# Kernel tuning notes

Hardware: AMD Instinct MI355X
Metric: run time of the kernel (lower is better)

The kernel has to match this reference:

```python
import jax, jax.numpy as jnp
import numpy as np


def setup_inputs() -> dict:
    key = jax.random.key(0)
    k1, k2, k3 = jax.random.split(key, 3)
    B, N, L, H, E = 4, 4, 1024, 8, 64
    queries = jax.random.normal(k1, (B, N, L, H, E), dtype=jnp.float32)
    keys = jax.random.normal(k2, (B, N, L, H, E), dtype=jnp.float32)
    values = jax.random.normal(k3, (B, N, L, H, E), dtype=jnp.float32)
    return {"queries": queries, "keys": keys, "values": values}


def reference(queries, keys, values):
    B, N, L, H, E = queries.shape
    S = values.shape[2]
    scale = 1.0 / jnp.sqrt(jnp.asarray(E, queries.dtype))
    # scores: [B, N, H, L, S]
    scores = jnp.einsum('bnlhe,bnshe->bnhls', queries, keys)
    # causal mask: True above the diagonal (future positions), broadcast over b,n,h
    causal = jnp.triu(jnp.ones((L, S), dtype=bool), k=1)
    scores = jnp.where(causal, -jnp.inf, scores)
    A = jax.nn.softmax(scale * scores, axis=-1)  # dropout p=0.0 -> identity
    V = jnp.einsum('bnhls,bnshd->bnlhd', A, values)
    return V
```

## Files before the change

### kernel.cpp

```cpp
#include <hip/hip_runtime.h>
#include <hip/hip_bf16.h>


typedef __bf16 bf16x8 __attribute__((ext_vector_type(8)));
typedef __bf16 bf16x4 __attribute__((ext_vector_type(4)));
typedef float  f32x4  __attribute__((ext_vector_type(4)));

#define SEQ 1024
#define ROWSTRIDE 512
#define LDSPAD 72

__device__ inline bf16x8 pack8(float4 a, float4 b) {
    bf16x8 f;
    f[0]=(__bf16)a.x; f[1]=(__bf16)a.y; f[2]=(__bf16)a.z; f[3]=(__bf16)a.w;
    f[4]=(__bf16)b.x; f[5]=(__bf16)b.y; f[6]=(__bf16)b.z; f[7]=(__bf16)b.w;
    return f;
}

__device__ inline bf16x8 pack8s(float4 a, float4 b, float s) {
    bf16x8 f;
    f[0]=(__bf16)(a.x*s); f[1]=(__bf16)(a.y*s); f[2]=(__bf16)(a.z*s); f[3]=(__bf16)(a.w*s);
    f[4]=(__bf16)(b.x*s); f[5]=(__bf16)(b.y*s); f[6]=(__bf16)(b.z*s); f[7]=(__bf16)(b.w*s);
    return f;
}

__device__ inline void lds_barrier() {
    asm volatile("s_waitcnt lgkmcnt(0)\n\ts_barrier" ::: "memory");
}

__global__ __launch_bounds__(256) void attn_fwd(
    const float* __restrict__ Qg,
    const float* __restrict__ Kg,
    const float* __restrict__ Vg,
    float* __restrict__ Og)
{
    __shared__ __bf16 Kds[64][LDSPAD];
    __shared__ __bf16 Vds[64][LDSPAD];
    __shared__ __bf16 Pds[2][4][16][LDSPAD];

    const int blk  = blockIdx.x;
    const int pr   = blk >> 7;
    const int head = blk & 127;
    const int h    = head & 7;
    const int bn   = head >> 3;
    const int qts[2] = { pr, 15 - pr };

    const int tid  = threadIdx.x;
    const int wave = tid >> 6;
    const int lane = tid & 63;
    const int quad = lane >> 4;
    const int l15  = lane & 15;

    const size_t base = (size_t)bn * SEQ * ROWSTRIDE + (size_t)h * 64;

    const float kscale = 0.125f * 1.44269504088896f;

    bf16x8 qa[2][2];
    int qrow[2];
    #pragma unroll
    for (int st = 0; st < 2; ++st) {
        qrow[st] = qts[st] * 64 + wave * 16;
        const float* qp = Qg + base + (size_t)(qrow[st] + l15) * ROWSTRIDE + quad * 8;
        #pragma unroll
        for (int t = 0; t < 2; ++t)
            qa[st][t] = pack8s(*(const float4*)(qp + t * 32),
                               *(const float4*)(qp + t * 32 + 4), kscale);
    }

    f32x4 o[2][4];
    float lsum[2];
    #pragma unroll
    for (int st = 0; st < 2; ++st) {
        #pragma unroll
        for (int e = 0; e < 4; ++e) o[st][e] = (f32x4){0.f, 0.f, 0.f, 0.f};
        lsum[st] = 0.f;
    }

    const int sr = tid >> 2, sc = (tid & 3) << 4;
    const int ve = tid & 63, vs = (tid >> 6) << 4;

    const int ntiles = qts[1] + 1;

    const float* kbase = Kg + base;
    const float* vbase = Vg + base;

    float4 kpre[4];
    float  vpre[16];
    {
        const float* kp = kbase + (size_t)sr * ROWSTRIDE + sc;
        #pragma unroll
        for (int i = 0; i < 4; ++i) kpre[i] = *(const float4*)(kp + i * 4);
        const float* vp = vbase + (size_t)vs * ROWSTRIDE + ve;
        #pragma unroll
        for (int j = 0; j < 16; ++j) vpre[j] = vp[(size_t)j * ROWSTRIDE];
    }

    for (int tile = 0; tile < ntiles; ++tile) {
        lds_barrier();

        *(bf16x8*)&Kds[sr][sc]     = pack8(kpre[0], kpre[1]);
        *(bf16x8*)&Kds[sr][sc + 8] = pack8(kpre[2], kpre[3]);
        {
            bf16x8 f0, f1;
            #pragma unroll
            for (int jj = 0; jj < 8; ++jj) { f0[jj] = (__bf16)vpre[jj]; f1[jj] = (__bf16)vpre[8 + jj]; }
            *(bf16x8*)&Vds[ve][vs]     = f0;
            *(bf16x8*)&Vds[ve][vs + 8] = f1;
        }

        if (tile + 1 < ntiles) {
            const int s0n = (tile + 1) * 64;
            const float* kp = kbase + (size_t)(s0n + sr) * ROWSTRIDE + sc;
            #pragma unroll
            for (int i = 0; i < 4; ++i) kpre[i] = *(const float4*)(kp + i * 4);
            const float* vp = vbase + (size_t)(s0n + vs) * ROWSTRIDE + ve;
            #pragma unroll
            for (int j = 0; j < 16; ++j) vpre[j] = vp[(size_t)j * ROWSTRIDE];
        }

        lds_barrier();

        #pragma unroll
        for (int st = 0; st < 2; ++st) {
            if (tile > qts[st]) continue;
            f32x4 sacc[4];
            #pragma unroll
            for (int c = 0; c < 4; ++c) {
                sacc[c] = (f32x4){0.f, 0.f, 0.f, 0.f};
                #pragma unroll
                for (int t = 0; t < 2; ++t) {
                    bf16x8 kb = *(const bf16x8*)&Kds[c * 16 + l15][t * 32 + quad * 8];
                    sacc[c] = __builtin_amdgcn_mfma_f32_16x16x32_bf16(kb, qa[st][t], sacc[c], 0, 0, 0);
                }
            }
            const bool diag = (tile == qts[st]);
            const int qin = wave * 16 + l15;
            float ls = 0.f;
            #pragma unroll
            for (int c = 0; c < 4; ++c) {
                bf16x4 pk;
                #pragma unroll
                for (int r = 0; r < 4; ++r) {
                    float p = __builtin_amdgcn_exp2f(sacc[c][r]);
                    if (diag && (c * 16 + quad * 4 + r > qin)) p = 0.f;
                    ls += p;
                    pk[r] = (__bf16)p;
                }
                *(bf16x4*)&Pds[st][wave][l15][c * 16 + quad * 4] = pk;
            }
            lsum[st] += ls;
        }

        asm volatile("s_waitcnt lgkmcnt(0)" ::: "memory");

        const bool both = (tile <= qts[0]);
        #pragma unroll
        for (int e = 0; e < 4; ++e) {
            #pragma unroll
            for (int t = 0; t < 2; ++t) {
                bf16x8 vb = *(const bf16x8*)&Vds[e * 16 + l15][t * 32 + quad * 8];
                if (both) {
                    bf16x8 pb0 = *(const bf16x8*)&Pds[0][wave][l15][t * 32 + quad * 8];
                    o[0][e] = __builtin_amdgcn_mfma_f32_16x16x32_bf16(vb, pb0, o[0][e], 0, 0, 0);
                }
                bf16x8 pb1 = *(const bf16x8*)&Pds[1][wave][l15][t * 32 + quad * 8];
                o[1][e] = __builtin_amdgcn_mfma_f32_16x16x32_bf16(vb, pb1, o[1][e], 0, 0, 0);
            }
        }
    }

    #pragma unroll
    for (int st = 0; st < 2; ++st) {
        float s = lsum[st];
        s += __shfl_xor(s, 16);
        s += __shfl_xor(s, 32);
        const float inv_l = 1.f / s;
        float* op = Og + base + (size_t)(qrow[st] + l15) * ROWSTRIDE + quad * 4;
        #pragma unroll
        for (int e = 0; e < 4; ++e) {
            float4 v;
            v.x = o[st][e][0] * inv_l;
            v.y = o[st][e][1] * inv_l;
            v.z = o[st][e][2] * inv_l;
            v.w = o[st][e][3] * inv_l;
            *(float4*)(op + e * 16) = v;
        }
    }
}

extern "C" void kernel_launch(void* const* d_in, const int* in_sizes, int n_in,
                              void* d_out, int out_size, void* d_ws, size_t ws_size,
                              hipStream_t stream) {
    const float* Qg = (const float*)d_in[0];
    const float* Kg = (const float*)d_in[1];
    const float* Vg = (const float*)d_in[2];
    float* Og = (float*)d_out;
    attn_fwd<<<dim3(1024), dim3(256), 0, stream>>>(Qg, Kg, Vg, Og);
}
```

Measured before the change: 163.5 us.

## Keep P in registers, double-buffer swizzled K/V LDS, use 16x16x16 MFMA for PV

```diff
diff --git a/kernel.cpp b/kernel.cpp
--- a/kernel.cpp
+++ b/kernel.cpp
@@ -5,10 +5,10 @@
 typedef __bf16 bf16x8 __attribute__((ext_vector_type(8)));
 typedef __bf16 bf16x4 __attribute__((ext_vector_type(4)));
 typedef float  f32x4  __attribute__((ext_vector_type(4)));
+typedef short  s16x4  __attribute__((ext_vector_type(4)));
 
 #define SEQ 1024
 #define ROWSTRIDE 512
-#define LDSPAD 72
 
 __device__ inline bf16x8 pack8(float4 a, float4 b) {
     bf16x8 f;
@@ -28,15 +28,14 @@
     asm volatile("s_waitcnt lgkmcnt(0)\n\ts_barrier" ::: "memory");
 }
 
-__global__ __launch_bounds__(256) void attn_fwd(
+__global__ __launch_bounds__(256, 4) void attn_fwd(
     const float* __restrict__ Qg,
     const float* __restrict__ Kg,
     const float* __restrict__ Vg,
     float* __restrict__ Og)
 {
-    __shared__ __bf16 Kds[64][LDSPAD];
-    __shared__ __bf16 Vds[64][LDSPAD];
-    __shared__ __bf16 Pds[2][4][16][LDSPAD];
+    __shared__ __bf16 Kds[2][64][64];
+    __shared__ __bf16 Vds[2][64][64];
 
     const int blk  = blockIdx.x;
     const int pr   = blk >> 7;
@@ -50,6 +49,7 @@
     const int lane = tid & 63;
     const int quad = lane >> 4;
     const int l15  = lane & 15;
+    const int swz  = l15 & 7;
 
     const size_t base = (size_t)bn * SEQ * ROWSTRIDE + (size_t)h * 64;
 
@@ -76,8 +76,8 @@
         lsum[st] = 0.f;
     }
 
-    const int sr = tid >> 2, sc = (tid & 3) << 4;
-    const int ve = tid & 63, vs = (tid >> 6) << 4;
+    const int sr = tid >> 2, cbk = (tid & 3) << 1;
+    const int ve = tid & 63, cbv = (tid >> 6) << 1;
 
     const int ntiles = qts[1] + 1;
 
@@ -87,39 +87,42 @@
     float4 kpre[4];
     float  vpre[16];
     {
-        const float* kp = kbase + (size_t)sr * ROWSTRIDE + sc;
+        const float* kp = kbase + (size_t)sr * ROWSTRIDE + (cbk << 3);
         #pragma unroll
         for (int i = 0; i < 4; ++i) kpre[i] = *(const float4*)(kp + i * 4);
-        const float* vp = vbase + (size_t)vs * ROWSTRIDE + ve;
+        const float* vp = vbase + (size_t)(cbv << 3) * ROWSTRIDE + ve;
         #pragma unroll
         for (int j = 0; j < 16; ++j) vpre[j] = vp[(size_t)j * ROWSTRIDE];
     }
 
     for (int tile = 0; tile < ntiles; ++tile) {
-        lds_barrier();
+        const int bb = tile & 1;
 
-        *(bf16x8*)&Kds[sr][sc]     = pack8(kpre[0], kpre[1]);
-        *(bf16x8*)&Kds[sr][sc + 8] = pack8(kpre[2], kpre[3]);
         {
+            const int rk = sr & 7;
+            *(bf16x8*)&Kds[bb][sr][(cbk ^ rk) << 3]       = pack8(kpre[0], kpre[1]);
+            *(bf16x8*)&Kds[bb][sr][((cbk + 1) ^ rk) << 3] = pack8(kpre[2], kpre[3]);
             bf16x8 f0, f1;
             #pragma unroll
             for (int jj = 0; jj < 8; ++jj) { f0[jj] = (__bf16)vpre[jj]; f1[jj] = (__bf16)vpre[8 + jj]; }
-            *(bf16x8*)&Vds[ve][vs]     = f0;
-            *(bf16x8*)&Vds[ve][vs + 8] = f1;
+            const int rv = ve & 7;
+            *(bf16x8*)&Vds[bb][ve][(cbv ^ rv) << 3]       = f0;
+            *(bf16x8*)&Vds[bb][ve][((cbv + 1) ^ rv) << 3] = f1;
         }
 
         if (tile + 1 < ntiles) {
-            const int s0n = (tile + 1) * 64;
-            const float* kp = kbase + (size_t)(s0n + sr) * ROWSTRIDE + sc;
+            const int s0n = (tile + 1) << 6;
+            const float* kp = kbase + (size_t)(s0n + sr) * ROWSTRIDE + (cbk << 3);
             #pragma unroll
             for (int i = 0; i < 4; ++i) kpre[i] = *(const float4*)(kp + i * 4);
-            const float* vp = vbase + (size_t)(s0n + vs) * ROWSTRIDE + ve;
+            const float* vp = vbase + (size_t)(s0n + (cbv << 3)) * ROWSTRIDE + ve;
             #pragma unroll
             for (int j = 0; j < 16; ++j) vpre[j] = vp[(size_t)j * ROWSTRIDE];
         }
 
         lds_barrier();
 
+        s16x4 pbs[2][4];
         #pragma unroll
         for (int st = 0; st < 2; ++st) {
             if (tile > qts[st]) continue;
@@ -129,7 +132,7 @@
                 sacc[c] = (f32x4){0.f, 0.f, 0.f, 0.f};
                 #pragma unroll
                 for (int t = 0; t < 2; ++t) {
-                    bf16x8 kb = *(const bf16x8*)&Kds[c * 16 + l15][t * 32 + quad * 8];
+                    bf16x8 kb = *(const bf16x8*)&Kds[bb][c * 16 + l15][((t * 4 + quad) ^ swz) << 3];
                     sacc[c] = __builtin_amdgcn_mfma_f32_16x16x32_bf16(kb, qa[st][t], sacc[c], 0, 0, 0);
                 }
             }
@@ -146,25 +149,21 @@
                     ls += p;
                     pk[r] = (__bf16)p;
                 }
-                *(bf16x4*)&Pds[st][wave][l15][c * 16 + quad * 4] = pk;
+                pbs[st][c] = __builtin_bit_cast(s16x4, pk);
             }
             lsum[st] += ls;
         }
 
-        asm volatile("s_waitcnt lgkmcnt(0)" ::: "memory");
-
         const bool both = (tile <= qts[0]);
+        const int qh = quad >> 1, ql = (quad & 1) << 2;
         #pragma unroll
         for (int e = 0; e < 4; ++e) {
             #pragma unroll
-            for (int t = 0; t < 2; ++t) {
-                bf16x8 vb = *(const bf16x8*)&Vds[e * 16 + l15][t * 32 + quad * 8];
-                if (both) {
-                    bf16x8 pb0 = *(const bf16x8*)&Pds[0][wave][l15][t * 32 + quad * 8];
-                    o[0][e] = __builtin_amdgcn_mfma_f32_16x16x32_bf16(vb, pb0, o[0][e], 0, 0, 0);
-                }
-                bf16x8 pb1 = *(const bf16x8*)&Pds[1][wave][l15][t * 32 + quad * 8];
-                o[1][e] = __builtin_amdgcn_mfma_f32_16x16x32_bf16(vb, pb1, o[1][e], 0, 0, 0);
+            for (int c = 0; c < 4; ++c) {
+                s16x4 vb = *(const s16x4*)&Vds[bb][e * 16 + l15][((((c << 1) + qh) ^ swz) << 3) + ql];
+                if (both)
+                    o[0][e] = __builtin_amdgcn_mfma_f32_16x16x16bf16_1k(vb, pbs[0][c], o[0][e], 0, 0, 0);
+                o[1][e] = __builtin_amdgcn_mfma_f32_16x16x16bf16_1k(vb, pbs[1][c], o[1][e], 0, 0, 0);
             }
         }
     }
```

Result: slower. 185.7 us (+13.6%).
